# Kernel tuning notes

Measured on AMD Instinct MI355X. Metric: run time of the kernel, lower is better.

Reference implementation:

```python
import jax, jax.numpy as jnp
import numpy as np

B, DIM, H, W = 8, 384, 64, 64
HEADS = 8
D = DIM // HEADS          # 48
D2 = D // 2               # 24
DU = D // 3 * 2           # 32 (ratio=3)


def setup_inputs() -> dict:
    key = jax.random.key(0)
    ks = jax.random.split(key, 12)
    s = lambda k, shape, scale=0.05: jax.random.normal(k, shape, jnp.float32) * scale
    return {
        "x": jax.random.normal(ks[0], (B, DIM, H, W), jnp.float32),
        "temperature": jnp.ones((HEADS, 1, 1), jnp.float32),
        "w_qkv": s(ks[1], (3 * DIM, DIM)),          # 1x1 conv, no bias
        "w_dw": s(ks[2], (3 * DIM, 1, 3, 3)),       # depthwise 3x3, groups=3*dim
        "w_proj": s(ks[3], (DIM, HEADS)),           # project_out 1x1
        "w_attn_r": s(ks[4], (1, D)),
        "w_v_r": s(ks[5], (D2, D)),
        "w_up1": s(ks[6], (DU, D2)),
        "b_up1": jnp.zeros((DU,), jnp.float32),
        "ln_w": jnp.ones((DU, HEADS, 1), jnp.float32),
        "ln_b": jnp.zeros((DU, HEADS, 1), jnp.float32),
        "w_up2": s(ks[7], (D, DU)),
        "b_up2": jnp.zeros((D,), jnp.float32),
        "w_attn_l": s(ks[8], (D2, D)),
        "w_v_l": s(ks[9], (D2, D)),
    }


def _qkv_attn(x, temperature, w_qkv, w_dw):
    # shared: qkv 1x1 conv -> depthwise 3x3 -> split, normalize, elementwise attn+softmax
    b, c, h, w = x.shape
    qkv = jnp.einsum('bchw,oc->bohw', x, w_qkv)
    qkv = jax.lax.conv_general_dilated(
        qkv, w_dw, (1, 1), 'SAME', feature_group_count=3 * c,
        dimension_numbers=('NCHW', 'OIHW', 'NCHW'))
    q, k, v = jnp.split(qkv, 3, axis=1)
    rs = lambda t: t.reshape(b, HEADS, D, h * w)  # b (head d) h w -> b head d (hw)
    q, k, v = rs(q), rs(k), rs(v)
    qn = q / jnp.maximum(jnp.linalg.norm(q, axis=-1, keepdims=True), 1e-12)
    kn = k / jnp.maximum(jnp.linalg.norm(k, axis=-1, keepdims=True), 1e-12)
    attn = jax.nn.softmax(qn * kn * temperature, axis=-1)  # [b, head, d, s]
    return attn, v


def _forward(x, temperature, w_qkv, w_dw, w_proj, w_attn_r, w_v_r,
             w_up1, b_up1, ln_w, ln_b, w_up2, b_up2, w_attn_l, w_v_l):
    b, c, h, w = x.shape
    attn, v = _qkv_attn(x, temperature, w_qkv, w_dw)

    # ---- spatial_pool (channel gating) ----
    input_x = jnp.einsum('bhds,od->bhos', v, w_v_r)                 # conv_v_right: [b,head,d2,s]
    cm = jax.nn.softmax(jnp.einsum('bhds,d->bhs', attn, w_attn_r[0]), axis=-1)  # conv_attn_right + softmax
    ctx = jnp.einsum('bhs,bhjs->bhj', cm, input_x)                  # [b,head,d2]
    ctx = ctx.transpose(0, 2, 1)[..., None]                         # [b, d2, head, 1]
    u = jnp.einsum('bchl,oc->bohl', ctx, w_up1) + b_up1[None, :, None, None]  # [b, DU, head, 1]
    mu = u.mean(axis=(1, 2, 3), keepdims=True)
    var = u.var(axis=(1, 2, 3), keepdims=True)
    u = (u - mu) / jnp.sqrt(var + 1e-5) * ln_w[None] + ln_b[None]   # LayerNorm([DU, 8, 1])
    u = jax.nn.relu(u)
    u = jnp.einsum('bchl,oc->bohl', u, w_up2) + b_up2[None, :, None, None]    # [b, D, head, 1]
    mask_ch = jax.nn.sigmoid(u).reshape(b, c, 1, 1)                 # view(b, head*D, 1, 1)
    out_channel = x * mask_ch

    # ---- channel_pool (spatial gating) ----
    g = jnp.einsum('bhds,od->bhos', attn, w_attn_l)                 # conv_attn_left: [b,head,d2,s]
    avg = jax.nn.softmax(g.mean(axis=-1), axis=-1)                  # avg-pool over s, softmax over d2
    theta = jnp.einsum('bhds,od->bhos', v, w_v_l)                   # conv_v_left: [b,head,d2,s]
    ctx2 = jnp.einsum('bhd,bhds->bhs', avg, theta)                  # matmul: [b,head,s]
    mask_sp = jax.nn.sigmoid(ctx2).reshape(b, HEADS, h, w)
    mask_sp = jnp.einsum('bchw,oc->bohw', mask_sp, w_proj)          # project_out
    out_spatial = x * mask_sp

    return out_spatial + out_channel


def reference(x, temperature, w_qkv, w_dw, w_proj, w_attn_r, w_v_r,
              w_up1, b_up1, ln_w, ln_b, w_up2, b_up2, w_attn_l, w_v_l):
    return _forward(x, temperature, w_qkv, w_dw, w_proj, w_attn_r, w_v_r,
                    w_up1, b_up1, ln_w, ln_b, w_up2, b_up2, w_attn_l, w_v_l)
```

## Files before the change

### kernel.cpp

```cpp
#include <hip/hip_runtime.h>
#include <math.h>


#define S4096 4096
#define C384  384
#define OC    1152

typedef unsigned short bfraw;
typedef unsigned int   u32;
typedef __attribute__((ext_vector_type(8))) short bf16x8;
typedef __attribute__((ext_vector_type(4))) float f32x4;

typedef __attribute__((address_space(3))) unsigned int lds_u32;
typedef const __attribute__((address_space(1))) unsigned int glb_u32;
__device__ __forceinline__ void gll16(const void* g, void* l) {
    __builtin_amdgcn_global_load_lds((glb_u32*)g, (lds_u32*)l, 16, 0, 0);
}

__device__ __forceinline__ bfraw f2bf(float f) {
    union { float f; u32 u; } c; c.f = f;
    u32 r = c.u + 0x7FFFu + ((c.u >> 16) & 1u);
    return (bfraw)(r >> 16);
}
__device__ __forceinline__ float bf2f(bfraw u) {
    union { u32 u; float f; } c; c.u = ((u32)u) << 16;
    return c.f;
}
__device__ __forceinline__ void unpack8(uint4 v, float* f) {
    f[0] = bf2f((bfraw)(v.x & 0xffff)); f[1] = bf2f((bfraw)(v.x >> 16));
    f[2] = bf2f((bfraw)(v.y & 0xffff)); f[3] = bf2f((bfraw)(v.y >> 16));
    f[4] = bf2f((bfraw)(v.z & 0xffff)); f[5] = bf2f((bfraw)(v.z >> 16));
    f[6] = bf2f((bfraw)(v.w & 0xffff)); f[7] = bf2f((bfraw)(v.w >> 16));
}
__device__ __forceinline__ uint4 pack8(const float* f) {
    union { bfraw us[8]; uint4 q; } p;
    #pragma unroll
    for (int i = 0; i < 8; i++) p.us[i] = f2bf(f[i]);
    return p.q;
}

__device__ __forceinline__ float blk_red(float v, float* s4, bool ismax) {
    #pragma unroll
    for (int off = 32; off; off >>= 1) {
        float o = __shfl_down(v, off, 64);
        v = ismax ? fmaxf(v, o) : (v + o);
    }
    __syncthreads();
    if ((threadIdx.x & 63) == 0) s4[threadIdx.x >> 6] = v;
    __syncthreads();
    return ismax ? fmaxf(fmaxf(s4[0], s4[1]), fmaxf(s4[2], s4[3]))
                 : ((s4[0] + s4[1]) + (s4[2] + s4[3]));
}

__global__ __launch_bounds__(256) void kA_prep(
    const float* __restrict__ w_qkv, bfraw* __restrict__ wF,
    const float* __restrict__ w_attn_l, const float* __restrict__ w_v_l,
    float* __restrict__ weff) {
    if (blockIdx.x == 216) {
        __shared__ float avg[24];
        const int tid = threadIdx.x;
        if (tid < 24) {
            float a = 0.f;
            for (int d = 0; d < 48; d++) a += w_attn_l[tid * 48 + d];
            avg[tid] = a * (1.f / 4096.f);
        }
        __syncthreads();
        if (tid == 0) {
            float M = -3.402823466e+38f;
            for (int o = 0; o < 24; o++) M = fmaxf(M, avg[o]);
            float S = 0.f;
            for (int o = 0; o < 24; o++) { avg[o] = __expf(avg[o] - M); S += avg[o]; }
            float inv = 1.f / S;
            for (int o = 0; o < 24; o++) avg[o] *= inv;
        }
        __syncthreads();
        if (tid < 48) {
            float a = 0.f;
            for (int o = 0; o < 24; o++) a += avg[o] * w_v_l[o * 48 + tid];
            weff[tid] = a;
        }
        return;
    }
    const int id = blockIdx.x * 256 + threadIdx.x;
    const int ob = id / 768, rem = id % 768;
    const int c = rem / 48, kb = rem % 48;
    const float* src = w_qkv + (size_t)(ob * 16 + c) * C384 + kb * 8;
    float f[8];
    *(float4*)f       = *(const float4*)src;
    *(float4*)(f + 4) = *(const float4*)(src + 4);
    *(uint4*)&wF[((size_t)(ob * 48 + kb) * 16 + c) * 8] = pack8(f);
}

__global__ __launch_bounds__(256) void kB_tr(
    const float* __restrict__ x, bfraw* __restrict__ xF, int b0) {
    const int cb = blockIdx.x, sb = blockIdx.y, bl = blockIdx.z;
    const int c0 = cb * 16, s0 = sb * 256;
    const int tid = threadIdx.x;
    __shared__ alignas(16) bfraw lt[16][264];
    {
        const int r = tid >> 4, seg = tid & 15;
        const float* src = x + ((size_t)(b0 + bl) * C384 + c0 + r) * S4096 + s0 + seg * 16;
        float f[16];
        #pragma unroll
        for (int i = 0; i < 4; i++) *(float4*)(f + i * 4) = *(const float4*)(src + i * 4);
        *(uint4*)&lt[r][seg * 16]     = pack8(f);
        *(uint4*)&lt[r][seg * 16 + 8] = pack8(f + 8);
    }
    __syncthreads();
    const int sbl = tid >> 4, c = tid & 15;
    bfraw* xFb = xF + (size_t)bl * S4096 * C384;
    #pragma unroll
    for (int kbl = 0; kbl < 2; kbl++) {
        union { bfraw us[8]; uint4 q; } p;
        #pragma unroll
        for (int j = 0; j < 8; j++) p.us[j] = lt[kbl * 8 + j][sbl * 16 + c];
        const size_t idx = (((size_t)((s0 >> 4) + sbl) * 48) + (c0 >> 3) + kbl) * 128 + c * 8;
        *(uint4*)&xFb[idx] = p.q;
    }
}

__global__ __launch_bounds__(256) void k1_gemm(
    const bfraw* __restrict__ wF, const bfraw* __restrict__ xF,
    bfraw* __restrict__ pre, int b0) {
    __shared__ alignas(16) bfraw smem[24576];
    const int tid = threadIdx.x;
    const int wave = tid >> 6, lane = tid & 63;
    const int sG = blockIdx.x, oT = blockIdx.y, bl = blockIdx.z;
    const bfraw* xFb = xF + (size_t)bl * S4096 * C384;

    const int c0_ = tid, c1_ = tid + 256;
    const int rb0 = c0_ >> 6, oc0 = (c0_ >> 4) & 3, rw0 = c0_ & 15;
    const int rb1 = c1_ >> 6, oc1 = (c1_ >> 4) & 3, rw1 = c1_ & 15;

    const bfraw* pA0 = wF + ((size_t)((oT * 8 + rb0) * 48 + oc0) * 16 + rw0) * 8;
    const bfraw* pA1 = wF + ((size_t)((oT * 8 + rb1) * 48 + oc1) * 16 + rw1) * 8;
    const bfraw* pB0 = xFb + ((size_t)((sG * 32 + rb0) * 48 + oc0) * 16 + rw0) * 8;
    const bfraw* pB1 = xFb + ((size_t)((sG * 32 + rb1) * 48 + oc1) * 16 + rw1) * 8;

    auto stage = [&](bfraw* dst, int ks, int st) {
        const int ko = ks * 512;
        const int so = st * 49152 + ko;
        gll16(pA0 + ko, dst + (size_t)c0_ * 8);
        gll16(pA1 + ko, dst + (size_t)c1_ * 8);
        gll16(pB0 + so, dst + 4096 + (size_t)c0_ * 8);
        gll16(pB1 + so, dst + 4096 + (size_t)c1_ * 8);
    };

    f32x4 acc[4][4];
    #pragma unroll
    for (int m = 0; m < 4; m++)
        #pragma unroll
        for (int n = 0; n < 4; n++) acc[m][n] = (f32x4){0, 0, 0, 0};

    const int wr = (wave >> 1) * 4;
    const int wc = (wave & 1) * 4;
    const int orow0 = oT * 128 + (wave >> 1) * 64 + (lane >> 4) * 4;
    bfraw* op = pre + (size_t)bl * OC * S4096;

    stage(smem,        0, 0);
    stage(smem + 8192, 1, 0);
    int ks_p = 2, st_p = 0, bp = 2;
    int ks_c = 0, st_c = 0, bi = 0;

    for (int i = 0; i < 48; ++i) {
        if (i < 47) asm volatile("s_waitcnt vmcnt(4)" ::: "memory");
        else        asm volatile("s_waitcnt vmcnt(0)" ::: "memory");
        __builtin_amdgcn_s_barrier();
        const bfraw* cb = smem + bi * 8192;
        bf16x8 af[4], bq[4];
        #pragma unroll
        for (int m = 0; m < 4; m++)
            af[m] = *(const bf16x8*)&cb[((wr + m) * 64 + lane) * 8];
        #pragma unroll
        for (int n = 0; n < 4; n++)
            bq[n] = *(const bf16x8*)&cb[4096 + ((wc + n) * 64 + lane) * 8];
        if (i < 46) {
            stage(smem + bp * 8192, ks_p, st_p);
            if (++ks_p == 12) { ks_p = 0; ++st_p; }
            bp = (bp == 2) ? 0 : bp + 1;
        }
        __builtin_amdgcn_s_setprio(1);
        #pragma unroll
        for (int m = 0; m < 4; m++)
            #pragma unroll
            for (int n = 0; n < 4; n++)
                acc[m][n] = __builtin_amdgcn_mfma_f32_16x16x32_bf16(af[m], bq[n], acc[m][n], 0, 0, 0);
        __builtin_amdgcn_s_setprio(0);
        if (++ks_c == 12) {
            const int scol0 = (sG * 4 + st_c) * 128 + (wave & 1) * 64 + (lane & 15);
            #pragma unroll
            for (int m = 0; m < 4; m++)
                #pragma unroll
                for (int n = 0; n < 4; n++)
                    #pragma unroll
                    for (int r = 0; r < 4; r++)
                        op[(size_t)(orow0 + m * 16 + r) * S4096 + scol0 + n * 16] = f2bf(acc[m][n][r]);
            #pragma unroll
            for (int m = 0; m < 4; m++)
                #pragma unroll
                for (int n = 0; n < 4; n++) acc[m][n] = (f32x4){0, 0, 0, 0};
            ks_c = 0; ++st_c;
        }
        bi = (bi == 2) ? 0 : bi + 1;
    }
}

__device__ __forceinline__ void stencil8(const bfraw* plane, const float* w9,
                                         int ypad, int k7, int x0, float* acc) {
    #pragma unroll
    for (int j = 0; j < 8; j++) acc[j] = 0.f;
    #pragma unroll
    for (int dy = 0; dy < 3; dy++) {
        uint4 rv = *(const uint4*)&plane[(ypad + dy) * 64 + x0];
        float r[8]; unpack8(rv, r);
        float lft = __shfl_up(r[7], 1);
        float rgt = __shfl_down(r[0], 1);
        if (k7 == 0) lft = 0.f;
        if (k7 == 7) rgt = 0.f;
        const float w0 = w9[dy*3], w1 = w9[dy*3+1], w2 = w9[dy*3+2];
        acc[0] += w0*lft + w1*r[0] + w2*r[1];
        #pragma unroll
        for (int j = 1; j < 7; j++) acc[j] += w0*r[j-1] + w1*r[j] + w2*r[j+1];
        acc[7] += w0*r[6] + w1*r[7] + w2*rgt;
    }
}

__global__ __launch_bounds__(256) void k2f(
    const bfraw* __restrict__ pre, const float* __restrict__ w_dw,
    const float* __restrict__ temperature,
    bfraw* __restrict__ av, int b0) {
    const int idx = blockIdx.x;
    const int bl  = blockIdx.y;
    const int h   = idx / 48;
    const int tid = threadIdx.x;
    __shared__ alignas(16) bfraw pl[3][66 * 64];
    __shared__ float s4[4];

    const size_t pbase = (size_t)bl * OC * S4096;
    #pragma unroll
    for (int p = 0; p < 3; p++) {
        const bfraw* src = pre + pbase + (size_t)(idx + p * C384) * S4096;
        uint4 a = *(const uint4*)&src[tid * 16];
        uint4 b = *(const uint4*)&src[tid * 16 + 8];
        int y = tid >> 2, xq = (tid & 3) * 16;
        *(uint4*)&pl[p][(y + 1) * 64 + xq]     = a;
        *(uint4*)&pl[p][(y + 1) * 64 + xq + 8] = b;
    }
    if (tid < 64) {
        #pragma unroll
        for (int p = 0; p < 3; p++) { pl[p][tid] = 0; pl[p][65 * 64 + tid] = 0; }
    }
    float wq[9], wk[9], wv[9];
    #pragma unroll
    for (int i = 0; i < 9; i++) {
        wq[i] = w_dw[idx * 9 + i];
        wk[i] = w_dw[(idx + C384) * 9 + i];
        wv[i] = w_dw[(idx + 768) * 9 + i];
    }
    __syncthreads();

    const int sid0 = tid,        y0 = sid0 >> 3, k70 = sid0 & 7, x00 = k70 * 8;
    const int sid1 = tid + 256,  y1 = sid1 >> 3, k71 = sid1 & 7, x01 = k71 * 8;
    float qo[16], ko[16], vo[16];
    stencil8(pl[0], wq, y0, k70, x00, qo);
    stencil8(pl[0], wq, y1, k71, x01, qo + 8);
    stencil8(pl[1], wk, y0, k70, x00, ko);
    stencil8(pl[1], wk, y1, k71, x01, ko + 8);
    stencil8(pl[2], wv, y0, k70, x00, vo);
    stencil8(pl[2], wv, y1, k71, x01, vo + 8);

    float sq = 0.f, sk = 0.f;
    #pragma unroll
    for (int i = 0; i < 16; i++) { sq += qo[i] * qo[i]; sk += ko[i] * ko[i]; }
    float Sq = blk_red(sq, s4, false);
    float Sk = blk_red(sk, s4, false);
    float scale = temperature[h] /
        (fmaxf(sqrtf(Sq), 1e-12f) * fmaxf(sqrtf(Sk), 1e-12f));
    float lm = -3.402823466e+38f;
    #pragma unroll
    for (int i = 0; i < 16; i++) { qo[i] = qo[i] * ko[i] * scale; lm = fmaxf(lm, qo[i]); }
    float M = blk_red(lm, s4, true);
    float ls = 0.f;
    #pragma unroll
    for (int i = 0; i < 16; i++) { qo[i] = __expf(qo[i] - M); ls += qo[i]; }
    float Z = blk_red(ls, s4, false);
    float invZ = 1.f / Z;
    #pragma unroll
    for (int i = 0; i < 16; i++) qo[i] *= invZ;

    bfraw* adst = av + ((size_t)bl * 768 + idx) * S4096;
    bfraw* vdst = av + ((size_t)bl * 768 + 384 + idx) * S4096;
    *(uint4*)&adst[y0 * 64 + x00] = pack8(qo);
    *(uint4*)&adst[y1 * 64 + x01] = pack8(qo + 8);
    *(uint4*)&vdst[y0 * 64 + x00] = pack8(vo);
    *(uint4*)&vdst[y1 * 64 + x01] = pack8(vo + 8);
}

__global__ __launch_bounds__(256) void k4a(
    const bfraw* __restrict__ av, const float* __restrict__ w_attn_r,
    const float* __restrict__ weff,
    bfraw* __restrict__ cmraw, bfraw* __restrict__ c2raw, int b0) {
    const int h = blockIdx.x, bl = blockIdx.y, st = blockIdx.z;
    const int b = b0 + bl;
    const int tid = threadIdx.x;
    __shared__ float swr[48], swf[48];
    if (tid < 48) { swr[tid] = w_attn_r[tid]; swf[tid] = weff[tid]; }
    __syncthreads();
    const int s_off = st * 1024 + tid * 4;
    const bfraw* abase = av + ((size_t)bl * 768 + h * 48) * S4096 + s_off;
    const bfraw* vbase = abase + (size_t)384 * S4096;
    float cmr[4] = {0,0,0,0}, c2[4] = {0,0,0,0};
    for (int d = 0; d < 48; d++) {
        uint2 ua = *(const uint2*)(abase + (size_t)d * S4096);
        uint2 uv = *(const uint2*)(vbase + (size_t)d * S4096);
        const float wr = swr[d], wf = swf[d];
        cmr[0] += bf2f((bfraw)(ua.x & 0xffff)) * wr;
        cmr[1] += bf2f((bfraw)(ua.x >> 16))    * wr;
        cmr[2] += bf2f((bfraw)(ua.y & 0xffff)) * wr;
        cmr[3] += bf2f((bfraw)(ua.y >> 16))    * wr;
        c2[0]  += bf2f((bfraw)(uv.x & 0xffff)) * wf;
        c2[1]  += bf2f((bfraw)(uv.x >> 16))    * wf;
        c2[2]  += bf2f((bfraw)(uv.y & 0xffff)) * wf;
        c2[3]  += bf2f((bfraw)(uv.y >> 16))    * wf;
    }
    const size_t o = ((size_t)(b * 8 + h)) * S4096 + s_off;
    union { bfraw us[4]; uint2 q; } pa, pb;
    #pragma unroll
    for (int j = 0; j < 4; j++) { pa.us[j] = f2bf(cmr[j]); pb.us[j] = f2bf(c2[j]); }
    *(uint2*)(cmraw + o) = pa.q;
    *(uint2*)(c2raw + o) = pb.q;
}

__global__ __launch_bounds__(256) void k4b(
    const bfraw* __restrict__ cmraw, const bfraw* __restrict__ c2raw,
    bfraw* __restrict__ cmb, bfraw* __restrict__ msp, int b0) {
    const int h = blockIdx.x, bl = blockIdx.y, b = b0 + bl;
    const int tid = threadIdx.x;
    __shared__ float s4[4];
    const size_t base = ((size_t)(b * 8 + h)) * S4096 + tid * 16;
    float v[16];
    { uint4 a = *(const uint4*)(cmraw + base), c = *(const uint4*)(cmraw + base + 8);
      unpack8(a, v); unpack8(c, v + 8); }
    float lm = -3.402823466e+38f;
    #pragma unroll
    for (int i = 0; i < 16; i++) lm = fmaxf(lm, v[i]);
    float M = blk_red(lm, s4, true);
    float ls = 0.f;
    #pragma unroll
    for (int i = 0; i < 16; i++) { v[i] = __expf(v[i] - M); ls += v[i]; }
    float Z = blk_red(ls, s4, false);
    float inv = 1.f / Z;
    #pragma unroll
    for (int i = 0; i < 16; i++) v[i] *= inv;
    *(uint4*)(cmb + base)     = pack8(v);
    *(uint4*)(cmb + base + 8) = pack8(v + 8);
    float sg[16];
    { uint4 a = *(const uint4*)(c2raw + base), c = *(const uint4*)(c2raw + base + 8);
      unpack8(a, sg); unpack8(c, sg + 8); }
    #pragma unroll
    for (int i = 0; i < 16; i++) sg[i] = 1.f / (1.f + __expf(-sg[i]));
    *(uint4*)(msp + base)     = pack8(sg);
    *(uint4*)(msp + base + 8) = pack8(sg + 8);
}

__global__ __launch_bounds__(256) void k5_vc(
    const bfraw* __restrict__ av, const bfraw* __restrict__ cmb,
    float* __restrict__ vc, int b0) {
    const int idx = blockIdx.x;
    const int bl = blockIdx.y, b = b0 + bl;
    const int h = idx / 48;
    const int tid = threadIdx.x;
    const bfraw* vr = av + ((size_t)bl * 768 + 384 + idx) * S4096 + tid * 16;
    const bfraw* cr = cmb + ((size_t)(b * 8 + h)) * S4096 + tid * 16;
    float vv[16], cc[16];
    { uint4 a = *(const uint4*)vr, c = *(const uint4*)(vr + 8); unpack8(a, vv); unpack8(c, vv + 8); }
    { uint4 a = *(const uint4*)cr, c = *(const uint4*)(cr + 8); unpack8(a, cc); unpack8(c, cc + 8); }
    float a = 0.f;
    #pragma unroll
    for (int i = 0; i < 16; i++) a += vv[i] * cc[i];
    __shared__ float s4[4];
    float S = blk_red(a, s4, false);
    if (tid == 0) vc[b * C384 + idx] = S;
}

__global__ __launch_bounds__(256) void k6_gate(
    const float* __restrict__ vc, const float* __restrict__ w_v_r,
    const float* __restrict__ w_up1, const float* __restrict__ b_up1,
    const float* __restrict__ ln_w, const float* __restrict__ ln_b,
    const float* __restrict__ w_up2, const float* __restrict__ b_up2,
    float* __restrict__ mch, int b0) {
    const int b = b0 + blockIdx.x;
    const int tid = threadIdx.x;
    __shared__ float s_vc[384], s_ctx[192], s_u[256], s4[4];
    for (int i = tid; i < 384; i += 256) s_vc[i] = vc[b * C384 + i];
    __syncthreads();
    if (tid < 192) {
        int hh = tid / 24, o = tid % 24;
        float a = 0.f;
        for (int d = 0; d < 48; d++) a += w_v_r[o * 48 + d] * s_vc[hh * 48 + d];
        s_ctx[hh * 24 + o] = a;
    }
    __syncthreads();
    float uval;
    {
        int o = tid >> 3, hh = tid & 7;
        float a = b_up1[o];
        for (int c = 0; c < 24; c++) a += w_up1[o * 24 + c] * s_ctx[hh * 24 + c];
        uval = a;
    }
    float mu  = blk_red(uval, s4, false) * (1.f / 256.f);
    float dv  = uval - mu;
    float var = blk_red(dv * dv, s4, false) * (1.f / 256.f);
    float un  = dv * rsqrtf(var + 1e-5f) * ln_w[tid] + ln_b[tid];
    s_u[tid] = fmaxf(un, 0.f);
    __syncthreads();
    for (int t = tid; t < 384; t += 256) {
        int o2 = t >> 3, hh = t & 7;
        float a = b_up2[o2];
        for (int o = 0; o < 32; o++) a += w_up2[o2 * 32 + o] * s_u[o * 8 + hh];
        mch[b * C384 + t] = 1.f / (1.f + __expf(-a));
    }
}

__global__ __launch_bounds__(256) void k7_out(
    const float* __restrict__ x, const float* __restrict__ w_proj,
    const float* __restrict__ mch, const bfraw* __restrict__ msp,
    float* __restrict__ out, int b0) {
    const int st = blockIdx.x, cg = blockIdx.y, bl = blockIdx.z;
    const int b = b0 + bl;
    const int tid = threadIdx.x;
    const int s0 = st * 256, c0 = cg * 48;
    __shared__ float s_msp[8][256];
    __shared__ float s_mch[48];
    __shared__ float s_wp[48][8];
    for (int i = tid; i < 2048; i += 256) {
        int hh = i >> 8, ss = i & 255;
        s_msp[hh][ss] = bf2f(msp[((size_t)(b * 8 + hh)) * S4096 + s0 + ss]);
    }
    if (tid < 48) s_mch[tid] = mch[b * C384 + c0 + tid];
    for (int i = tid; i < 384; i += 256)
        s_wp[i >> 3][i & 7] = w_proj[(size_t)(c0 + (i >> 3)) * 8 + (i & 7)];
    __syncthreads();

    const int cl = tid >> 6;
    const int s4i = (tid & 63) * 4;
    float4 m[8];
    #pragma unroll
    for (int hh = 0; hh < 8; hh++) m[hh] = *(const float4*)&s_msp[hh][s4i];

    #pragma unroll 4
    for (int j = 0; j < 12; j++) {
        const int cloc = j * 4 + cl;
        const int c = c0 + cloc;
        const float base = s_mch[cloc];
        float4 a = {base, base, base, base};
        #pragma unroll
        for (int hh = 0; hh < 8; hh++) {
            const float wp = s_wp[cloc][hh];
            a.x += wp * m[hh].x; a.y += wp * m[hh].y;
            a.z += wp * m[hh].z; a.w += wp * m[hh].w;
        }
        const size_t o = ((size_t)b * C384 + c) * S4096 + s0 + s4i;
        float4 xv = *(const float4*)(x + o);
        a.x *= xv.x; a.y *= xv.y; a.z *= xv.z; a.w *= xv.w;
        *(float4*)(out + o) = a;
    }
}

extern "C" void kernel_launch(void* const* d_in, const int* in_sizes, int n_in,
                              void* d_out, int out_size, void* d_ws, size_t ws_size,
                              hipStream_t stream) {
    const float* x        = (const float*)d_in[0];
    const float* temp     = (const float*)d_in[1];
    const float* w_qkv    = (const float*)d_in[2];
    const float* w_dw     = (const float*)d_in[3];
    const float* w_proj   = (const float*)d_in[4];
    const float* w_attn_r = (const float*)d_in[5];
    const float* w_v_r    = (const float*)d_in[6];
    const float* w_up1    = (const float*)d_in[7];
    const float* b_up1    = (const float*)d_in[8];
    const float* ln_w     = (const float*)d_in[9];
    const float* ln_b     = (const float*)d_in[10];
    const float* w_up2    = (const float*)d_in[11];
    const float* b_up2    = (const float*)d_in[12];
    const float* w_attn_l = (const float*)d_in[13];
    const float* w_v_l    = (const float*)d_in[14];
    float* out = (float*)d_out;
    char* ws = (char*)d_ws;

    size_t off = 0;
    auto alloc = [&](size_t bytes) {
        size_t o = off; off = (off + bytes + 255) & ~(size_t)255; return o;
    };
    bfraw* cmraw = (bfraw*)(ws + alloc((size_t)64 * S4096 * 2));
    bfraw* c2raw = (bfraw*)(ws + alloc((size_t)64 * S4096 * 2));
    bfraw* cmb   = (bfraw*)(ws + alloc((size_t)64 * S4096 * 2));
    bfraw* msp   = (bfraw*)(ws + alloc((size_t)64 * S4096 * 2));
    float* vc    = (float*)(ws + alloc(3072 * 4));
    float* mch   = (float*)(ws + alloc(3072 * 4));
    float* weff  = (float*)(ws + alloc(256));
    bfraw* wF    = (bfraw*)(ws + alloc((size_t)55296 * 16));
    const size_t big_xF  = (size_t)S4096 * C384 * 2;
    const size_t big_pre = (size_t)OC * S4096 * 2;
    const size_t big_av  = (size_t)768 * S4096 * 2;
    int nb = (ws_size >= off + 8 * (big_xF + big_pre + big_av)) ? 8 : 1;
    bfraw* xF  = (bfraw*)(ws + alloc((size_t)nb * big_xF));
    bfraw* pre = (bfraw*)(ws + alloc((size_t)nb * big_pre));
    bfraw* av  = (bfraw*)(ws + alloc((size_t)nb * big_av));

    kA_prep<<<217, 256, 0, stream>>>(w_qkv, wF, w_attn_l, w_v_l, weff);
    for (int b0 = 0; b0 < 8; b0 += nb) {
        kB_tr<<<dim3(24, 16, nb), 256, 0, stream>>>(x, xF, b0);
        k1_gemm<<<dim3(8, 9, nb), 256, 0, stream>>>(wF, xF, pre, b0);
        k2f<<<dim3(384, nb), 256, 0, stream>>>(pre, w_dw, temp, av, b0);
        k4a<<<dim3(8, nb, 4), 256, 0, stream>>>(av, w_attn_r, weff, cmraw, c2raw, b0);
        k4b<<<dim3(8, nb), 256, 0, stream>>>(cmraw, c2raw, cmb, msp, b0);
        k5_vc<<<dim3(384, nb), 256, 0, stream>>>(av, cmb, vc, b0);
        k6_gate<<<dim3(nb), 256, 0, stream>>>(vc, w_v_r, w_up1, b_up1,
                                              ln_w, ln_b, w_up2, b_up2, mch, b0);
        k7_out<<<dim3(16, 8, nb), 256, 0, stream>>>(x, w_proj, mch, msp, out, b0);
    }
}
```

Baseline: 136.9 us.

## Split QKV GEMM into one tile per block and load weights directly to registers

The QKV projection GEMM previously had each block loop over four spatial tiles with a triple-buffered LDS pipeline for both weights and activations. Now each block computes a single 128x128 output tile, so the grid grows fourfold (32x9xnb). The activation tile is double-buffered in LDS via global_load_lds, while weight fragments are read straight from global memory into registers and prefetched one k-step ahead. This trades deeper pipelining for more blocks to fill the CUs, at the cost of a barrier every k-step and more global weight traffic.

```diff
diff --git a/kernel.cpp b/kernel.cpp
--- a/kernel.cpp
+++ b/kernel.cpp
@@ -122,87 +122,80 @@
 __global__ __launch_bounds__(256) void k1_gemm(
     const bfraw* __restrict__ wF, const bfraw* __restrict__ xF,
     bfraw* __restrict__ pre, int b0) {
-    __shared__ alignas(16) bfraw smem[24576];
+    __shared__ alignas(16) bfraw b_sm[2][4096];
     const int tid = threadIdx.x;
     const int wave = tid >> 6, lane = tid & 63;
-    const int sG = blockIdx.x, oT = blockIdx.y, bl = blockIdx.z;
+    const int sT = blockIdx.x, oT = blockIdx.y, bl = blockIdx.z;
     const bfraw* xFb = xF + (size_t)bl * S4096 * C384;
 
     const int c0_ = tid, c1_ = tid + 256;
     const int rb0 = c0_ >> 6, oc0 = (c0_ >> 4) & 3, rw0 = c0_ & 15;
     const int rb1 = c1_ >> 6, oc1 = (c1_ >> 4) & 3, rw1 = c1_ & 15;
-
-    const bfraw* pA0 = wF + ((size_t)((oT * 8 + rb0) * 48 + oc0) * 16 + rw0) * 8;
-    const bfraw* pA1 = wF + ((size_t)((oT * 8 + rb1) * 48 + oc1) * 16 + rw1) * 8;
-    const bfraw* pB0 = xFb + ((size_t)((sG * 32 + rb0) * 48 + oc0) * 16 + rw0) * 8;
-    const bfraw* pB1 = xFb + ((size_t)((sG * 32 + rb1) * 48 + oc1) * 16 + rw1) * 8;
-
-    auto stage = [&](bfraw* dst, int ks, int st) {
-        const int ko = ks * 512;
-        const int so = st * 49152 + ko;
-        gll16(pA0 + ko, dst + (size_t)c0_ * 8);
-        gll16(pA1 + ko, dst + (size_t)c1_ * 8);
-        gll16(pB0 + so, dst + 4096 + (size_t)c0_ * 8);
-        gll16(pB1 + so, dst + 4096 + (size_t)c1_ * 8);
-    };
-
-    f32x4 acc[4][4];
-    #pragma unroll
-    for (int m = 0; m < 4; m++)
-        #pragma unroll
-        for (int n = 0; n < 4; n++) acc[m][n] = (f32x4){0, 0, 0, 0};
+    const bfraw* pB0 = xFb + ((size_t)((sT * 8 + rb0) * 48 + oc0) * 16 + rw0) * 8;
+    const bfraw* pB1 = xFb + ((size_t)((sT * 8 + rb1) * 48 + oc1) * 16 + rw1) * 8;
 
     const int wr = (wave >> 1) * 4;
     const int wc = (wave & 1) * 4;
-    const int orow0 = oT * 128 + (wave >> 1) * 64 + (lane >> 4) * 4;
-    bfraw* op = pre + (size_t)bl * OC * S4096;
-
-    stage(smem,        0, 0);
-    stage(smem + 8192, 1, 0);
-    int ks_p = 2, st_p = 0, bp = 2;
-    int ks_c = 0, st_c = 0, bi = 0;
-
-    for (int i = 0; i < 48; ++i) {
-        if (i < 47) asm volatile("s_waitcnt vmcnt(4)" ::: "memory");
-        else        asm volatile("s_waitcnt vmcnt(0)" ::: "memory");
-        __builtin_amdgcn_s_barrier();
-        const bfraw* cb = smem + bi * 8192;
-        bf16x8 af[4], bq[4];
-        #pragma unroll
-        for (int m = 0; m < 4; m++)
-            af[m] = *(const bf16x8*)&cb[((wr + m) * 64 + lane) * 8];
+    const int l15 = lane & 15, kq = lane >> 4;
+
+    const bfraw* pA[4];
+    #pragma unroll
+    for (int m = 0; m < 4; m++)
+        pA[m] = wF + (((size_t)(oT * 8 + wr + m) * 48 + kq) * 16 + l15) * 8;
+
+    f32x4 acc[4][4];
+    #pragma unroll
+    for (int m = 0; m < 4; m++)
+        #pragma unroll
+        for (int n = 0; n < 4; n++) acc[m][n] = (f32x4){0, 0, 0, 0};
+
+    gll16(pB0, &b_sm[0][(size_t)c0_ * 8]);
+    gll16(pB1, &b_sm[0][(size_t)c1_ * 8]);
+    bf16x8 a_cur[4];
+    #pragma unroll
+    for (int m = 0; m < 4; m++) a_cur[m] = *(const bf16x8*)(pA[m]);
+    __syncthreads();
+
+    #pragma unroll
+    for (int ks = 0; ks < 12; ks++) {
+        const bfraw* cb = b_sm[ks & 1];
+        bf16x8 bq[4];
         #pragma unroll
         for (int n = 0; n < 4; n++)
-            bq[n] = *(const bf16x8*)&cb[4096 + ((wc + n) * 64 + lane) * 8];
-        if (i < 46) {
-            stage(smem + bp * 8192, ks_p, st_p);
-            if (++ks_p == 12) { ks_p = 0; ++st_p; }
-            bp = (bp == 2) ? 0 : bp + 1;
+            bq[n] = *(const bf16x8*)&cb[((wc + n) * 64 + lane) * 8];
+        bf16x8 a_nxt[4];
+        if (ks < 11) {
+            bfraw* nb = (bfraw*)b_sm[(ks & 1) ^ 1];
+            gll16(pB0 + (ks + 1) * 512, nb + (size_t)c0_ * 8);
+            gll16(pB1 + (ks + 1) * 512, nb + (size_t)c1_ * 8);
+            #pragma unroll
+            for (int m = 0; m < 4; m++)
+                a_nxt[m] = *(const bf16x8*)(pA[m] + (ks + 1) * 512);
         }
         __builtin_amdgcn_s_setprio(1);
         #pragma unroll
         for (int m = 0; m < 4; m++)
             #pragma unroll
             for (int n = 0; n < 4; n++)
-                acc[m][n] = __builtin_amdgcn_mfma_f32_16x16x32_bf16(af[m], bq[n], acc[m][n], 0, 0, 0);
+                acc[m][n] = __builtin_amdgcn_mfma_f32_16x16x32_bf16(a_cur[m], bq[n], acc[m][n], 0, 0, 0);
         __builtin_amdgcn_s_setprio(0);
-        if (++ks_c == 12) {
-            const int scol0 = (sG * 4 + st_c) * 128 + (wave & 1) * 64 + (lane & 15);
+        if (ks < 11) {
             #pragma unroll
-            for (int m = 0; m < 4; m++)
-                #pragma unroll
-                for (int n = 0; n < 4; n++)
-                    #pragma unroll
-                    for (int r = 0; r < 4; r++)
-                        op[(size_t)(orow0 + m * 16 + r) * S4096 + scol0 + n * 16] = f2bf(acc[m][n][r]);
+            for (int m = 0; m < 4; m++) a_cur[m] = a_nxt[m];
+        }
+        __syncthreads();
+    }
+
+    bfraw* op = pre + (size_t)bl * OC * S4096;
+    const int orow0 = oT * 128 + (wave >> 1) * 64 + (lane >> 4) * 4;
+    const int scol0 = sT * 128 + (wave & 1) * 64 + l15;
+    #pragma unroll
+    for (int m = 0; m < 4; m++)
+        #pragma unroll
+        for (int n = 0; n < 4; n++)
             #pragma unroll
-            for (int m = 0; m < 4; m++)
-                #pragma unroll
-                for (int n = 0; n < 4; n++) acc[m][n] = (f32x4){0, 0, 0, 0};
-            ks_c = 0; ++st_c;
-        }
-        bi = (bi == 2) ? 0 : bi + 1;
-    }
+            for (int r = 0; r < 4; r++)
+                op[(size_t)(orow0 + m * 16 + r) * S4096 + scol0 + n * 16] = f2bf(acc[m][n][r]);
 }
 
 __device__ __forceinline__ void stencil8(const bfraw* plane, const float* w9,
@@ -511,7 +504,7 @@
     kA_prep<<<217, 256, 0, stream>>>(w_qkv, wF, w_attn_l, w_v_l, weff);
     for (int b0 = 0; b0 < 8; b0 += nb) {
         kB_tr<<<dim3(24, 16, nb), 256, 0, stream>>>(x, xF, b0);
-        k1_gemm<<<dim3(8, 9, nb), 256, 0, stream>>>(wF, xF, pre, b0);
+        k1_gemm<<<dim3(32, 9, nb), 256, 0, stream>>>(wF, xF, pre, b0);
         k2f<<<dim3(384, nb), 256, 0, stream>>>(pre, w_dw, temp, av, b0);
         k4a<<<dim3(8, nb, 4), 256, 0, stream>>>(av, w_attn_r, weff, cmraw, c2raw, b0);
         k4b<<<dim3(8, nb), 256, 0, stream>>>(cmraw, c2raw, cmb, msp, b0);
```

Measured after the change: 126.4 us (median of 2 runs). -7.6%, faster.
